# Optimization experiments

Measured on AMD Instinct MI355X. Metric: run time of the kernel, lower is better.

## Reference

```python
import jax, jax.numpy as jnp
from jax import lax
import numpy as np

B, T, F, K = 64, 512, 1024, 64


def setup_inputs() -> dict:
    key = jax.random.key(0)
    ks = jax.random.split(key, 7)
    text_vec = jax.random.normal(ks[0], (B, T, F), dtype=jnp.float32)
    # variable-length mask; first timestep always on (torchcrf requirement)
    lengths = jax.random.randint(ks[1], (B,), T // 2, T + 1)
    mask = jnp.arange(T)[None, :] < lengths[:, None]  # [B,T] bool
    W = jax.random.normal(ks[2], (K, F), dtype=jnp.float32) * 0.02
    b = jnp.zeros((K,), dtype=jnp.float32)
    start_transitions = jax.random.uniform(ks[3], (K,), minval=-0.1, maxval=0.1)
    end_transitions = jax.random.uniform(ks[4], (K,), minval=-0.1, maxval=0.1)
    transitions = jax.random.uniform(ks[5], (K, K), minval=-0.1, maxval=0.1)
    return dict(text_vec=text_vec, mask=mask, W=W, b=b,
                start_transitions=start_transitions,
                end_transitions=end_transitions,
                transitions=transitions)


def _viterbi_decode(emission, mask, start, end, trans):
    """emission [N,T,K] float, mask [N,T] bool -> best tags [N,T] int32.
    Faithful masked Viterbi (torchcrf semantics); padded positions carry the
    last valid tag forward."""
    N, Tlen, Ktags = emission.shape
    score0 = start[None, :] + emission[:, 0]  # [N,K]
    idx_id = jnp.broadcast_to(jnp.arange(Ktags), (N, Ktags))

    def step(score, xs):
        e_t, m_t = xs  # [N,K], [N]
        cand = score[:, :, None] + trans[None, :, :] + e_t[:, None, :]  # [N,Kprev,Knext]
        new_score = jnp.max(cand, axis=1)
        best_prev = jnp.argmax(cand, axis=1)  # [N,K]
        new_score = jnp.where(m_t[:, None], new_score, score)
        best_prev = jnp.where(m_t[:, None], best_prev, idx_id)
        return new_score, best_prev

    xs = (jnp.swapaxes(emission[:, 1:], 0, 1), mask[:, 1:].T)  # time-major
    final_score, hist = lax.scan(step, score0, xs)  # hist [T-1,N,K]
    final_score = final_score + end[None, :]
    last_tag = jnp.argmax(final_score, axis=-1)  # [N]

    def back(tag, h_t):
        prev = jnp.take_along_axis(h_t, tag[:, None], axis=1)[:, 0]
        return prev, tag

    first_tag, tags_rest = lax.scan(back, last_tag, hist, reverse=True)
    tags = jnp.concatenate([first_tag[None, :], tags_rest], axis=0).T  # [N,T]
    return tags.astype(jnp.int32)


def reference(text_vec, mask, W, b, start_transitions, end_transitions, transitions):
    # cal_emission: Linear then reshape [B,T,K] -> [B,1,T,K]
    em = jnp.einsum('btf,kf->btk', text_vec, W) + b  # [B,T,K]
    emission = em[:, None, :, :]  # [B,1,T,K]
    # decode: flatten the singleton dim and run Viterbi
    em_flat = emission.reshape(-1, T, K)  # [B*1,T,K]
    mask_flat = jnp.broadcast_to(mask[:, None, :], (B, 1, T)).reshape(-1, T)
    pred = _viterbi_decode(em_flat, mask_flat, start_transitions,
                           end_transitions, transitions)
    pred = pred.reshape(B, 1, T)
    return emission, pred
```

## Files before the change

### kernel.cpp

```cpp
#include <hip/hip_runtime.h>
#include <hip/hip_bf16.h>

#define BB 64
#define TT 512
#define FF 1024
#define KK 64

typedef unsigned char uchar;

#define BM 64
#define BF 64
#define LDA 68

__global__ __launch_bounds__(256)
void emission_kernel(const float* __restrict__ X, const float* __restrict__ W,
                     const float* __restrict__ bias, float* __restrict__ em)
{
    __shared__ float As[BF][LDA];
    __shared__ float Bs[BF][LDA];
    const int tid = threadIdx.x;
    const int row0 = blockIdx.x * BM;
    const int tm = tid & 15;
    const int tn = tid >> 4;
    const int lq = tid & 15;
    const int lr = tid >> 4;

    float acc[4][4];
#pragma unroll
    for (int i = 0; i < 4; ++i)
#pragma unroll
        for (int jj = 0; jj < 4; ++jj) acc[i][jj] = 0.f;

    for (int f0 = 0; f0 < FF; f0 += BF) {
#pragma unroll
        for (int p = 0; p < 4; ++p) {
            const int r = p * 16 + lr;
            float4 a = *(const float4*)(X + (size_t)(row0 + r) * FF + f0 + lq * 4);
            As[lq * 4 + 0][r] = a.x;
            As[lq * 4 + 1][r] = a.y;
            As[lq * 4 + 2][r] = a.z;
            As[lq * 4 + 3][r] = a.w;
            float4 w = *(const float4*)(W + (size_t)r * FF + f0 + lq * 4);
            Bs[lq * 4 + 0][r] = w.x;
            Bs[lq * 4 + 1][r] = w.y;
            Bs[lq * 4 + 2][r] = w.z;
            Bs[lq * 4 + 3][r] = w.w;
        }
        __syncthreads();
#pragma unroll
        for (int f = 0; f < BF; ++f) {
            float4 a = *(const float4*)&As[f][tm * 4];
            float4 b = *(const float4*)&Bs[f][tn * 4];
            acc[0][0] += a.x * b.x; acc[0][1] += a.x * b.y; acc[0][2] += a.x * b.z; acc[0][3] += a.x * b.w;
            acc[1][0] += a.y * b.x; acc[1][1] += a.y * b.y; acc[1][2] += a.y * b.z; acc[1][3] += a.y * b.w;
            acc[2][0] += a.z * b.x; acc[2][1] += a.z * b.y; acc[2][2] += a.z * b.z; acc[2][3] += a.z * b.w;
            acc[3][0] += a.w * b.x; acc[3][1] += a.w * b.y; acc[3][2] += a.w * b.z; acc[3][3] += a.w * b.w;
        }
        __syncthreads();
    }

    const float4 b4 = *(const float4*)(bias + tn * 4);
#pragma unroll
    for (int i = 0; i < 4; ++i) {
        float4 o;
        o.x = acc[i][0] + b4.x;
        o.y = acc[i][1] + b4.y;
        o.z = acc[i][2] + b4.z;
        o.w = acc[i][3] + b4.w;
        *(float4*)(em + (size_t)(row0 + tm * 4 + i) * KK + tn * 4) = o;
    }
}

#define VSTEP(EV, TIDX) do {                                                   \
    const float* sp = &sbuf[(TIDX) & 1][0];                                    \
    float m_;                                                                  \
    _Pragma("unroll")                                                          \
    for (int c = 0; c < 8; ++c) {                                              \
        const float4 s0 = *(const float4*)(sp + c * 8);                        \
        const float4 s1 = *(const float4*)(sp + c * 8 + 4);                    \
        const float v0 = s0.x + tc[c * 8 + 0];                                 \
        const float v1 = s0.y + tc[c * 8 + 1];                                 \
        const float v2 = s0.z + tc[c * 8 + 2];                                 \
        const float v3 = s0.w + tc[c * 8 + 3];                                 \
        const float v4 = s1.x + tc[c * 8 + 4];                                 \
        const float v5 = s1.y + tc[c * 8 + 5];                                 \
        const float v6 = s1.z + tc[c * 8 + 6];                                 \
        const float v7 = s1.w + tc[c * 8 + 7];                                 \
        const float ma = fmaxf(fmaxf(v0, v1), v2);                 \
        const float mb = fmaxf(fmaxf(v3, v4), v5);                             \
        const float mc = fmaxf(fmaxf(v6, v7), ma);                             \
        const float w_ = fmaxf(mb, mc);                                        \
        m_ = (c == 0) ? w_ : fmaxf(m_, w_);                                    \
    }                                                                          \
    score = m_ + (EV);                                                         \
    sbuf[((TIDX) + 1) & 1][j] = score;       \
    sb[(size_t)(TIDX) * KK + j] = score;                                       \
} while (0)

#define RLANE(I) __uint_as_float((unsigned)__builtin_amdgcn_readlane((int)__float_as_uint(score), (I)))

__global__ __launch_bounds__(64)
__attribute__((amdgpu_waves_per_eu(1, 1)))
void viterbi_fwd(const float* __restrict__ em, const void* __restrict__ maskp,
                 const float* __restrict__ startT, const float* __restrict__ endT,
                 const float* __restrict__ trans, float* __restrict__ shist,
                 int* __restrict__ btarr)
{
    __shared__ float sbuf[2][KK];

    const int b = blockIdx.x;
    const int j = threadIdx.x;

    const uchar* m8 = (const uchar*)maskp;
    const int* m32 = (const int*)maskp;
    const bool u8m = (m8[1] != 0);

    int myc;
    if (u8m) {
        const uint2 mv = *(const uint2*)(m8 + (size_t)b * TT + j * 8);
        const unsigned s4 = (mv.x & 0x01010101u) + (mv.y & 0x01010101u);
        myc = (int)((s4 * 0x01010101u) >> 24);
    } else {
        const int* mp = m32 + (size_t)b * TT + j * 8;
        const int4 a = *(const int4*)mp;
        const int4 c = *(const int4*)(mp + 4);
        myc = (a.x != 0) + (a.y != 0) + (a.z != 0) + (a.w != 0)
            + (c.x != 0) + (c.y != 0) + (c.z != 0) + (c.w != 0);
    }
#pragma unroll
    for (int o = 1; o < 64; o <<= 1) myc += __shfl_xor(myc, o, 64);
    const int len = myc;

    float tc[KK];
#pragma unroll
    for (int i = 0; i < KK; ++i) tc[i] = trans[i * KK + j];
#pragma unroll
    for (int i = 0; i < KK; ++i) asm volatile("" : "+v"(tc[i]));

    const float* emb = em + (size_t)b * TT * KK;
    float* sb = shist + (size_t)b * TT * KK;

    float score = startT[j] + emb[j];
    sb[j] = score;
    sbuf[1][j] = score;

    float eA = emb[1 * KK + j];
    float eB = emb[2 * KK + j];
    float eC = emb[3 * KK + j];
    float eD = emb[4 * KK + j];

    int t = 1;
    for (; t + 3 < len; t += 4) {
        VSTEP(eA, t);     eA = emb[(size_t)((t + 4 < TT) ? t + 4 : TT - 1) * KK + j];
        VSTEP(eB, t + 1); eB = emb[(size_t)((t + 5 < TT) ? t + 5 : TT - 1) * KK + j];
        VSTEP(eC, t + 2); eC = emb[(size_t)((t + 6 < TT) ? t + 6 : TT - 1) * KK + j];
        VSTEP(eD, t + 3); eD = emb[(size_t)((t + 7 < TT) ? t + 7 : TT - 1) * KK + j];
    }
    for (; t < len; ++t) {
        VSTEP(eA, t);
        eA = eB; eB = eC; eC = eD;
    }

    score += endT[j];
    float bm = -__builtin_inff();
    int bt = 0;
#pragma unroll
    for (int i = 0; i < KK; ++i) {
        const float si = RLANE(i);
        if (si > bm) { bm = si; bt = i; }
    }
    if (j == 0) btarr[b] = bt;
}

__global__ __launch_bounds__(256)
void hist_kernel(const float* __restrict__ em, const void* __restrict__ maskp,
                 const float* __restrict__ trans, const float* __restrict__ shist,
                 uchar* __restrict__ histg)
{
    const int tid = threadIdx.x;
    const int bid = blockIdx.x;
    const int b = bid >> 6;
    const int t0 = (bid & 63) * 8;

    __shared__ float tl[64][65];
    __shared__ float srow[8][64];

    const uchar* m8 = (const uchar*)maskp;
    const int* m32 = (const int*)maskp;
    const bool u8m = (m8[1] != 0);

#pragma unroll
    for (int p = 0; p < 16; ++p) {
        const int idx = p * 256 + tid;
        tl[idx >> 6][idx & 63] = trans[idx];
    }
#pragma unroll
    for (int p = 0; p < 2; ++p) {
        const int idx = p * 256 + tid;
        const int r = idx >> 6, i2 = idx & 63;
        const int ts = t0 - 1 + r;
        srow[r][i2] = (ts >= 0) ? shist[((size_t)b * TT + ts) * KK + i2] : 0.f;
    }
    __syncthreads();

    const int j = tid & 63;
    const int tq = tid >> 6;

#pragma unroll
    for (int half = 0; half < 2; ++half) {
        const int toff = tq * 2 + half;
        const int t = t0 + toff;
        if (t == 0) continue;
        const int mt = u8m ? (int)m8[b * TT + t] : m32[b * TT + t];
        uchar hv;
        if (!mt) {
            hv = (uchar)j;
        } else {
            const float e = em[((size_t)b * TT + t) * KK + j];
            const float* sr = &srow[toff][0];
            float bm = -__builtin_inff();
            int bi = 0;
#pragma unroll 16
            for (int i = 0; i < KK; ++i) {
                const float cand = (sr[i] + tl[i][j]) + e;
                if (cand > bm) { bm = cand; bi = i; }
            }
            hv = (uchar)bi;
        }
        histg[((size_t)b * TT + t) * KK + j] = hv;
    }
}

__global__ __launch_bounds__(256)
void viterbi_bt(const uchar* __restrict__ histg, const int* __restrict__ btarr,
                float* __restrict__ pred)
{
    const int b = blockIdx.x;
    const int tid = threadIdx.x;
    const int w = tid >> 6;
    const int j = tid & 63;

    __shared__ uchar hist[TT][KK];
    __shared__ uchar hypo[8][64][64];

    const uint4* src = (const uint4*)(histg + (size_t)b * TT * KK);
    uint4* dst = (uint4*)&hist[0][0];
#pragma unroll
    for (int p = 0; p < 8; ++p) dst[p * 256 + tid] = src[p * 256 + tid];
    __syncthreads();

    const int bt = btarr[b];

#pragma unroll
    for (int ss = 0; ss < 2; ++ss) {
        const int s = w * 2 + ss;
        int tag = j;
        if (s == 7) {
            hypo[7][63][j] = (uchar)j;
            for (int t = TT - 1; t >= 7 * 64 + 1; --t) {
                tag = hist[t][tag];
                hypo[7][t - 1 - 7 * 64][j] = (uchar)tag;
            }
        } else {
            for (int t = (s + 1) * 64; t >= s * 64 + 1; --t) {
                tag = hist[t][tag];
                hypo[s][t - 1 - s * 64][j] = (uchar)tag;
            }
        }
    }
    __syncthreads();

    int rows_[8];
    rows_[7] = bt;
#pragma unroll
    for (int s = 6; s >= 0; --s) rows_[s] = hypo[s + 1][0][rows_[s + 1]];

    float* pb = pred + (size_t)b * TT;
#pragma unroll
    for (int ss = 0; ss < 2; ++ss) {
        const int s = w * 2 + ss;
        pb[s * 64 + j] = (float)hypo[s][j][rows_[s]];
    }
}

__global__ __launch_bounds__(256)
void viterbi_kernel(const float* __restrict__ em, const void* __restrict__ maskp,
                    const float* __restrict__ startT, const float* __restrict__ endT,
                    const float* __restrict__ trans, float* __restrict__ pred)
{
    const int b = blockIdx.x;
    const int tid = threadIdx.x;
    const int w = tid >> 6;
    const int j = tid & 63;

    __shared__ uchar hist[TT][KK];
    __shared__ uchar hypo[8][64][64];
    __shared__ int bt_sh;

    const uchar* m8 = (const uchar*)maskp;
    const int* m32 = (const int*)maskp;
    const bool u8m = (m8[1] != 0);

    if (w == 0) {
        float tc[KK];
#pragma unroll
        for (int i = 0; i < KK; ++i) tc[i] = trans[i * KK + j];

        const float* emb = em + (size_t)b * TT * KK;
        float score = startT[j] + emb[j];
        const float endv = endT[j];

        float e_cur = emb[KK + j];
        int   m_cur = u8m ? (int)m8[b * TT + 1] : m32[b * TT + 1];

        int t = 1;
        for (; t < TT; ++t) {
            const int tn2 = (t + 1 < TT) ? (t + 1) : (TT - 1);
            const float e_next = emb[(size_t)tn2 * KK + j];
            const int   m_next = u8m ? (int)m8[b * TT + tn2] : m32[b * TT + tn2];
            if (!m_cur) break;
            float m = -__builtin_inff();
            int idx = 0;
#pragma unroll
            for (int i = 0; i < KK; ++i) {
                const float si = __uint_as_float(__builtin_amdgcn_readlane(__float_as_uint(score), i));
                const float v = (si + tc[i]) + e_cur;
                if (v > m) { m = v; idx = i; }
            }
            score = m;
            hist[t][j] = (uchar)idx;
            e_cur = e_next; m_cur = m_next;
        }
        for (; t < TT; ++t) hist[t][j] = (uchar)j;

        score += endv;
        float bm = -__builtin_inff();
        int bt = 0;
#pragma unroll
        for (int i = 0; i < KK; ++i) {
            const float si = __uint_as_float(__builtin_amdgcn_readlane(__float_as_uint(score), i));
            if (si > bm) { bm = si; bt = i; }
        }
        if (j == 0) bt_sh = bt;
    }
    __syncthreads();

#pragma unroll
    for (int ss = 0; ss < 2; ++ss) {
        const int s = w * 2 + ss;
        int tag = j;
        if (s == 7) {
            hypo[7][63][j] = (uchar)j;
            for (int t = TT - 1; t >= 7 * 64 + 1; --t) {
                tag = hist[t][tag];
                hypo[7][t - 1 - 7 * 64][j] = (uchar)tag;
            }
        } else {
            for (int t = (s + 1) * 64; t >= s * 64 + 1; --t) {
                tag = hist[t][tag];
                hypo[s][t - 1 - s * 64][j] = (uchar)tag;
            }
        }
    }
    __syncthreads();

    const int bt = bt_sh;
    int rows_[8];
    rows_[7] = bt;
#pragma unroll
    for (int s = 6; s >= 0; --s) rows_[s] = hypo[s + 1][0][rows_[s + 1]];

    float* pb = pred + (size_t)b * TT;
#pragma unroll
    for (int ss = 0; ss < 2; ++ss) {
        const int s = w * 2 + ss;
        pb[s * 64 + j] = (float)hypo[s][j][rows_[s]];
    }
}

extern "C" void kernel_launch(void* const* d_in, const int* in_sizes, int n_in,
                              void* d_out, int out_size, void* d_ws, size_t ws_size,
                              hipStream_t stream) {
    const float* X      = (const float*)d_in[0];
    const void*  mask   = d_in[1];
    const float* W      = (const float*)d_in[2];
    const float* bias   = (const float*)d_in[3];
    const float* startT = (const float*)d_in[4];
    const float* endT   = (const float*)d_in[5];
    const float* trans  = (const float*)d_in[6];

    float* em   = (float*)d_out;
    float* pred = (float*)d_out + (size_t)BB * TT * KK;

    emission_kernel<<<(BB * TT) / BM, 256, 0, stream>>>(X, W, bias, em);

    const size_t SH_BYTES = (size_t)BB * TT * KK * sizeof(float);
    const size_t HI_BYTES = (size_t)BB * TT * KK;
    const size_t NEED = SH_BYTES + HI_BYTES + 256;

    if (ws_size >= NEED) {
        float* shist = (float*)d_ws;
        uchar* histg = (uchar*)d_ws + SH_BYTES;
        int*   btarr = (int*)((uchar*)d_ws + SH_BYTES + HI_BYTES);
        viterbi_fwd<<<BB, 64, 0, stream>>>(em, mask, startT, endT, trans, shist, btarr);
        hist_kernel<<<BB * 64, 256, 0, stream>>>(em, mask, trans, shist, histg);
        viterbi_bt<<<BB, 256, 0, stream>>>(histg, btarr, pred);
    } else {
        viterbi_kernel<<<BB, 256, 0, stream>>>(em, mask, startT, endT, trans, pred);
    }
}
```

Baseline: 243.3 us.

## Transpose W and restructure emission GEMM; pack Viterbi adds into float2

Adds a kernel that transposes W into workspace, plus a new emission GEMM. In the new GEMM each thread computes one row and 16 output columns, X is staged transposed in LDS, and the W^T rows are read as wave-uniform 16-float vectors. Separately, the Viterbi forward step stores transitions as float2 pairs so the compiler can emit packed float adds. The new path needs extra workspace and an extra launch, and it gives up the previous register-tiled 4x4 GEMM design.

Result: faster. 233.5 us (-4.0%).

```diff
diff --git a/kernel.cpp b/kernel.cpp
--- a/kernel.cpp
+++ b/kernel.cpp
@@ -7,6 +7,71 @@
 #define KK 64
 
 typedef unsigned char uchar;
+typedef float float2v __attribute__((ext_vector_type(2)));
+typedef float wv16 __attribute__((ext_vector_type(16)));
+
+__global__ __launch_bounds__(256)
+void wt_kernel(const float* __restrict__ W, float* __restrict__ WT)
+{
+    const int idx = blockIdx.x * 256 + threadIdx.x;
+    const int c = idx >> 10;
+    const int f = idx & 1023;
+    WT[(size_t)f * KK + c] = W[idx];
+}
+
+__global__ __launch_bounds__(256)
+void emission2_kernel(const float* __restrict__ X, const float* __restrict__ WT,
+                      const float* __restrict__ bias, float* __restrict__ em)
+{
+    __shared__ float As[64][65];
+    const int tid = threadIdx.x;
+    const int row0 = blockIdx.x * 64;
+    const int lane = tid & 63;
+    const int cw = 16 * (int)__builtin_amdgcn_readfirstlane(tid >> 6);
+
+    const int sr = tid >> 2;
+    const int sq = tid & 3;
+
+    float acc[16];
+#pragma unroll
+    for (int c = 0; c < 16; ++c) acc[c] = 0.f;
+
+    for (int f0 = 0; f0 < FF; f0 += 64) {
+#pragma unroll
+        for (int p = 0; p < 4; ++p) {
+            const int fl = p * 16 + sq * 4;
+            const float4 a = *(const float4*)(X + (size_t)(row0 + sr) * FF + f0 + fl);
+            As[fl + 0][sr] = a.x;
+            As[fl + 1][sr] = a.y;
+            As[fl + 2][sr] = a.z;
+            As[fl + 3][sr] = a.w;
+        }
+        __syncthreads();
+#pragma unroll 16
+        for (int f = 0; f < 64; ++f) {
+            const float av = As[f][lane];
+            const wv16 bv = *(const wv16*)(WT + (size_t)(f0 + f) * KK + cw);
+#pragma unroll
+            for (int c = 0; c < 16; ++c) acc[c] = fmaf(av, bv[c], acc[c]);
+        }
+        __syncthreads();
+    }
+
+    const float4 b0 = *(const float4*)(bias + cw);
+    const float4 b1 = *(const float4*)(bias + cw + 4);
+    const float4 b2 = *(const float4*)(bias + cw + 8);
+    const float4 b3 = *(const float4*)(bias + cw + 12);
+    float* outp = em + (size_t)(row0 + lane) * KK + cw;
+    float4 o;
+    o.x = acc[0] + b0.x;  o.y = acc[1] + b0.y;  o.z = acc[2] + b0.z;  o.w = acc[3] + b0.w;
+    *(float4*)(outp + 0) = o;
+    o.x = acc[4] + b1.x;  o.y = acc[5] + b1.y;  o.z = acc[6] + b1.z;  o.w = acc[7] + b1.w;
+    *(float4*)(outp + 4) = o;
+    o.x = acc[8] + b2.x;  o.y = acc[9] + b2.y;  o.z = acc[10] + b2.z; o.w = acc[11] + b2.w;
+    *(float4*)(outp + 8) = o;
+    o.x = acc[12] + b3.x; o.y = acc[13] + b3.y; o.z = acc[14] + b3.z; o.w = acc[15] + b3.w;
+    *(float4*)(outp + 12) = o;
+}
 
 #define BM 64
 #define BF 64
@@ -72,23 +137,17 @@
 }
 
 #define VSTEP(EV, TIDX) do {                                                   \
-    const float* sp = &sbuf[(TIDX) & 1][0];                                    \
+    const float2v* sp2 = (const float2v*)&sbuf[(TIDX) & 1][0];                 \
     float m_;                                                                  \
     _Pragma("unroll")                                                          \
     for (int c = 0; c < 8; ++c) {                                              \
-        const float4 s0 = *(const float4*)(sp + c * 8);                        \
-        const float4 s1 = *(const float4*)(sp + c * 8 + 4);                    \
-        const float v0 = s0.x + tc[c * 8 + 0];                                 \
-        const float v1 = s0.y + tc[c * 8 + 1];                                 \
-        const float v2 = s0.z + tc[c * 8 + 2];                                 \
-        const float v3 = s0.w + tc[c * 8 + 3];                                 \
-        const float v4 = s1.x + tc[c * 8 + 4];                                 \
-        const float v5 = s1.y + tc[c * 8 + 5];                                 \
-        const float v6 = s1.z + tc[c * 8 + 6];                                 \
-        const float v7 = s1.w + tc[c * 8 + 7];                                 \
-        const float ma = fmaxf(fmaxf(v0, v1), v2);                 \
-        const float mb = fmaxf(fmaxf(v3, v4), v5);                             \
-        const float mc = fmaxf(fmaxf(v6, v7), ma);                             \
+        const float2v p0 = sp2[c * 4 + 0] + tc2[c * 4 + 0];                    \
+        const float2v p1 = sp2[c * 4 + 1] + tc2[c * 4 + 1];                    \
+        const float2v p2 = sp2[c * 4 + 2] + tc2[c * 4 + 2];                    \
+        const float2v p3 = sp2[c * 4 + 3] + tc2[c * 4 + 3];                    \
+        const float ma = fmaxf(fmaxf(p0.x, p0.y), p1.x);           \
+        const float mb = fmaxf(fmaxf(p1.y, p2.x), p2.y);                       \
+        const float mc = fmaxf(fmaxf(p3.x, p3.y), ma);                         \
         const float w_ = fmaxf(mb, mc);                                        \
         m_ = (c == 0) ? w_ : fmaxf(m_, w_);                                    \
     }                                                                          \
@@ -131,11 +190,14 @@
     for (int o = 1; o < 64; o <<= 1) myc += __shfl_xor(myc, o, 64);
     const int len = myc;
 
-    float tc[KK];
-#pragma unroll
-    for (int i = 0; i < KK; ++i) tc[i] = trans[i * KK + j];
-#pragma unroll
-    for (int i = 0; i < KK; ++i) asm volatile("" : "+v"(tc[i]));
+    float2v tc2[32];
+#pragma unroll
+    for (int i = 0; i < 32; ++i) {
+        tc2[i].x = trans[(2 * i) * KK + j];
+        tc2[i].y = trans[(2 * i + 1) * KK + j];
+    }
+#pragma unroll
+    for (int i = 0; i < 32; ++i) asm volatile("" : "+v"(tc2[i]));
 
     const float* emb = em + (size_t)b * TT * KK;
     float* sb = shist + (size_t)b * TT * KK;
@@ -392,20 +454,23 @@
     float* em   = (float*)d_out;
     float* pred = (float*)d_out + (size_t)BB * TT * KK;
 
-    emission_kernel<<<(BB * TT) / BM, 256, 0, stream>>>(X, W, bias, em);
-
     const size_t SH_BYTES = (size_t)BB * TT * KK * sizeof(float);
     const size_t HI_BYTES = (size_t)BB * TT * KK;
-    const size_t NEED = SH_BYTES + HI_BYTES + 256;
+    const size_t WT_OFF   = SH_BYTES + HI_BYTES + 256;
+    const size_t NEED = WT_OFF + (size_t)KK * FF * sizeof(float);
 
     if (ws_size >= NEED) {
         float* shist = (float*)d_ws;
         uchar* histg = (uchar*)d_ws + SH_BYTES;
         int*   btarr = (int*)((uchar*)d_ws + SH_BYTES + HI_BYTES);
+        float* WT    = (float*)((uchar*)d_ws + WT_OFF);
+        wt_kernel<<<256, 256, 0, stream>>>(W, WT);
+        emission2_kernel<<<(BB * TT) / 64, 256, 0, stream>>>(X, WT, bias, em);
         viterbi_fwd<<<BB, 64, 0, stream>>>(em, mask, startT, endT, trans, shist, btarr);
         hist_kernel<<<BB * 64, 256, 0, stream>>>(em, mask, trans, shist, histg);
         viterbi_bt<<<BB, 256, 0, stream>>>(histg, btarr, pred);
     } else {
+        emission_kernel<<<(BB * TT) / BM, 256, 0, stream>>>(X, W, bias, em);
         viterbi_kernel<<<BB, 256, 0, stream>>>(em, mask, startT, endT, trans, pred);
     }
 }
```
